# Performance work log

Measured on AMD Instinct MI355X. Metric: run time of the kernel, lower is better.

The kernel has to match this reference:

```python
import jax, jax.numpy as jnp
import numpy as np

B, S, D_IN, D_OUT = 2, 2048, 2048, 2048
NH, NKV = 16, 4
HD = D_OUT // NH          # 128
GS = NH // NKV            # 4


def _rope_tables(seq_len, head_dim, base=10000.0):
    inv = 1.0 / (base ** (np.arange(0, head_dim, 2, dtype=np.float32) / head_dim))
    t = np.arange(seq_len, dtype=np.float32)
    ang = np.outer(t, inv)                       # [S, HD/2]
    ang = np.concatenate([ang, ang], axis=-1)    # [S, HD]
    return jnp.asarray(np.cos(ang)), jnp.asarray(np.sin(ang))


def setup_inputs() -> dict:
    key = jax.random.key(0)
    ks = jax.random.split(key, 5)
    x = jax.random.normal(ks[0], (B, S, D_IN), dtype=jnp.float32)
    Wq = jax.random.normal(ks[1], (D_IN, D_OUT), dtype=jnp.float32) * 0.02
    Wk = jax.random.normal(ks[2], (D_IN, NKV * HD), dtype=jnp.float32) * 0.02
    Wv = jax.random.normal(ks[3], (D_IN, NKV * HD), dtype=jnp.float32) * 0.02
    Wo = jax.random.normal(ks[4], (D_OUT, D_OUT), dtype=jnp.float32) * 0.02
    cos, sin = _rope_tables(S, HD)
    return {"x": x, "Wq": Wq, "Wk": Wk, "Wv": Wv, "Wo": Wo, "cos": cos, "sin": sin}


def _apply_rope(t, cos, sin):
    # t: [b, h, s, hd]; cos/sin: [s, hd]
    hd = t.shape[-1]
    t1, t2 = t[..., : hd // 2], t[..., hd // 2:]
    rot = jnp.concatenate([-t2, t1], axis=-1)
    return t * cos[None, None, :, :] + rot * sin[None, None, :, :]


def reference(x, Wq, Wk, Wv, Wo, cos, sin):
    b, s, _ = x.shape
    q = (x @ Wq).reshape(b, s, NH, HD).transpose(0, 2, 1, 3)    # [b, nh, s, hd]
    k = (x @ Wk).reshape(b, s, NKV, HD).transpose(0, 2, 1, 3)   # [b, nkv, s, hd]
    v = (x @ Wv).reshape(b, s, NKV, HD).transpose(0, 2, 1, 3)
    q = _apply_rope(q, cos, sin)
    k = _apply_rope(k, cos, sin)
    # GQA: repeat_interleave kv heads to match query heads
    k = jnp.repeat(k, GS, axis=1)                               # [b, nh, s, hd]
    v = jnp.repeat(v, GS, axis=1)
    att = jnp.einsum("bhqd,bhkd->bhqk", q, k) / jnp.sqrt(jnp.float32(HD))
    causal = jnp.triu(jnp.ones((s, s), dtype=bool), k=1)         # True above diag
    att = jnp.where(causal[None, None, :, :], -jnp.inf, att)
    att = jax.nn.softmax(att, axis=-1)
    ctx = jnp.einsum("bhqk,bhkd->bhqd", att, v)                  # [b, nh, s, hd]
    ctx = ctx.transpose(0, 2, 1, 3).reshape(b, s, NH * HD)
    return ctx @ Wo
```

## Files before the change

### kernel.cpp

```cpp
#include <hip/hip_runtime.h>

#define B_ 2
#define S_ 2048
#define DIN 2048
#define DOUT 2048
#define NH 16
#define NKV 4
#define HD 128
#define QS3 3072
#define KOFF 2048
#define VOFF 2560
#define SMAX 14.0f
#define NQT 16

typedef __bf16 bf16x8 __attribute__((ext_vector_type(8)));
typedef float f32x4 __attribute__((ext_vector_type(4)));

__device__ inline unsigned short f2bf(float f) {
  union { float f; unsigned int u; } v; v.f = f;
  unsigned int r = v.u + 0x7fffu + ((v.u >> 16) & 1u);
  return (unsigned short)(r >> 16);
}
__device__ inline unsigned short f2bf_trunc(float f) {
  return (unsigned short)(__builtin_bit_cast(unsigned int, f) >> 16);
}
__device__ inline float bf2f(unsigned short h) {
  union { unsigned int u; float f; } v; v.u = ((unsigned int)h) << 16;
  return v.f;
}
__device__ inline float exp2_fast(float x) {
  float r;
  asm("v_exp_f32 %0, %1\n\ts_nop 1" : "=v"(r) : "v"(x));
  return r;
}

__device__ inline void gl_lds16(const void* g, void* l) {
  __builtin_amdgcn_global_load_lds(
      (const __attribute__((address_space(1))) void*)g,
      (__attribute__((address_space(3))) void*)l, 16, 0, 0);
}

template <int N>
__device__ inline float rrot(float v) {
  return __builtin_bit_cast(float,
      __builtin_amdgcn_update_dpp(0, __builtin_bit_cast(int, v), 0x120 | N, 0xF, 0xF, true));
}
__device__ inline float rsum16(float v) {
  v += rrot<1>(v); v += rrot<2>(v); v += rrot<4>(v); v += rrot<8>(v);
  return v;
}

__global__ __launch_bounds__(256) void cast_bf16_k(const float* __restrict__ in,
                                                   unsigned short* __restrict__ out, int n4) {
  int i = blockIdx.x * 256 + threadIdx.x;
  if (i >= n4) return;
  float4 v = ((const float4*)in)[i];
  ushort4 o;
  o.x = f2bf(v.x); o.y = f2bf(v.y); o.z = f2bf(v.z); o.w = f2bf(v.w);
  ((ushort4*)out)[i] = o;
}

__global__ void transpose_cast_k(const float* __restrict__ W, unsigned short* __restrict__ Wt,
                                 int K, int N, float scale) {
  __shared__ float tile[32][33];
  int n0 = blockIdx.x * 32, k0 = blockIdx.y * 32;
  int tx = threadIdx.x, ty = threadIdx.y;
  #pragma unroll
  for (int j = 0; j < 32; j += 8)
    tile[ty + j][tx] = W[(size_t)(k0 + ty + j) * N + n0 + tx];
  __syncthreads();
  #pragma unroll
  for (int j = 0; j < 32; j += 8)
    Wt[(size_t)(n0 + ty + j) * K + k0 + tx] = f2bf(tile[tx][ty + j] * scale);
}

__global__ void transpose_v_k(const unsigned short* __restrict__ QKV,
                              unsigned short* __restrict__ Vt) {
  __shared__ unsigned short t[32][33];
  int c0 = blockIdx.x * 32, s0 = blockIdx.y * 32, b = blockIdx.z;
  int tx = threadIdx.x, ty = threadIdx.y;
  #pragma unroll
  for (int j = 0; j < 32; j += 8)
    t[ty + j][tx] = QKV[(size_t)(b * S_ + s0 + ty + j) * QS3 + VOFF + c0 + tx];
  __syncthreads();
  #pragma unroll
  for (int j = 0; j < 32; j += 8)
    Vt[(size_t)(b * (NKV * HD) + c0 + ty + j) * S_ + s0 + tx] = t[tx][ty + j];
}

template <int OUT_BF16>
__global__ __launch_bounds__(256) void gemm_bt_k(const unsigned short* __restrict__ A,
                                                 const unsigned short* __restrict__ Bt,
                                                 void* __restrict__ Cout,
                                                 int M, int N, int K) {
  __shared__ unsigned short As[128 * 32];
  __shared__ unsigned short Bs[128 * 32];
  int tid = threadIdx.x;
  int lane = tid & 63, wave = tid >> 6;
  int wy = wave >> 1, wx = wave & 1;
  int rowA0 = blockIdx.x * 128, rowB0 = blockIdx.y * 128;
  int m16 = lane & 15, quad = lane >> 4;
  int xq = (m16 >> 1) & 3;
  f32x4 acc[4][4] = {};

  int r0 = tid >> 2, l0 = (tid & 3) ^ ((r0 >> 1) & 3);
  int c1 = 256 + tid;
  int r1 = c1 >> 2, l1 = (c1 & 3) ^ ((r1 >> 1) & 3);
  const unsigned short* pa0 = A  + (size_t)(rowA0 + r0) * K + l0 * 8;
  const unsigned short* pa1 = A  + (size_t)(rowA0 + r1) * K + l1 * 8;
  const unsigned short* pb0 = Bt + (size_t)(rowB0 + r0) * K + l0 * 8;
  const unsigned short* pb1 = Bt + (size_t)(rowB0 + r1) * K + l1 * 8;
  unsigned short* la = As + (tid & 192) * 8;
  unsigned short* lb = Bs + (tid & 192) * 8;

  for (int k0 = 0; k0 < K; k0 += 32) {
    __syncthreads();
    gl_lds16(pa0 + k0, la);
    gl_lds16(pb0 + k0, lb);
    gl_lds16(pa1 + k0, la + 2048);
    gl_lds16(pb1 + k0, lb + 2048);
    __syncthreads();
    bf16x8 af[4], bfr[4];
    #pragma unroll
    for (int i = 0; i < 4; ++i)
      af[i] = *(const bf16x8*)(As + (wy * 64 + i * 16 + m16) * 32 + (quad ^ xq) * 8);
    #pragma unroll
    for (int j = 0; j < 4; ++j)
      bfr[j] = *(const bf16x8*)(Bs + (wx * 64 + j * 16 + m16) * 32 + (quad ^ xq) * 8);
    #pragma unroll
    for (int i = 0; i < 4; ++i)
      #pragma unroll
      for (int j = 0; j < 4; ++j)
        acc[i][j] = __builtin_amdgcn_mfma_f32_16x16x32_bf16(af[i], bfr[j], acc[i][j], 0, 0, 0);
  }

  #pragma unroll
  for (int i = 0; i < 4; ++i) {
    #pragma unroll
    for (int j = 0; j < 4; ++j) {
      int row = rowA0 + wy * 64 + i * 16 + quad * 4;
      int col = rowB0 + wx * 64 + j * 16 + m16;
      #pragma unroll
      for (int r = 0; r < 4; ++r) {
        float v = acc[i][j][r];
        if (OUT_BF16)
          ((unsigned short*)Cout)[(size_t)(row + r) * N + col] = f2bf(v);
        else
          ((float*)Cout)[(size_t)(row + r) * N + col] = v;
      }
    }
  }
}

__global__ __launch_bounds__(256) void rope_k(unsigned short* __restrict__ T,
                                              const float* __restrict__ cosT,
                                              const float* __restrict__ sinT,
                                              int stride, int off, int lognh) {
  int idx = blockIdx.x * 256 + threadIdx.x;
  int d = (idx & 15) * 4;
  int t = idx >> 4;
  int nh = 1 << lognh;
  int h = t & (nh - 1);
  int bs = t >> lognh;
  int s = bs & (S_ - 1);
  unsigned short* p = T + (size_t)bs * stride + off + h * HD;
  ushort4 a = *(ushort4*)(p + d);
  ushort4 bq = *(ushort4*)(p + 64 + d);
  float4 c = *(const float4*)(cosT + s * HD + d);
  float4 sn = *(const float4*)(sinT + s * HD + d);
  ushort4 o1, o2;
  o1.x = f2bf(bf2f(a.x) * c.x - bf2f(bq.x) * sn.x);
  o2.x = f2bf(bf2f(bq.x) * c.x + bf2f(a.x) * sn.x);
  o1.y = f2bf(bf2f(a.y) * c.y - bf2f(bq.y) * sn.y);
  o2.y = f2bf(bf2f(bq.y) * c.y + bf2f(a.y) * sn.y);
  o1.z = f2bf(bf2f(a.z) * c.z - bf2f(bq.z) * sn.z);
  o2.z = f2bf(bf2f(bq.z) * c.z + bf2f(a.z) * sn.z);
  o1.w = f2bf(bf2f(a.w) * c.w - bf2f(bq.w) * sn.w);
  o2.w = f2bf(bf2f(bq.w) * c.w + bf2f(a.w) * sn.w);
  *(ushort4*)(p + d) = o1;
  *(ushort4*)(p + 64 + d) = o2;
}

#define LDP 40
__global__ __launch_bounds__(256) void flash_k(const unsigned short* __restrict__ QKV,
                                               const unsigned short* __restrict__ Vt,
                                               unsigned short* __restrict__ ctx,
                                               unsigned short* __restrict__ Opart,
                                               float* __restrict__ lpart,
                                               int CHUNK, int units_per_bh) {
  __shared__ unsigned short Ks[2][32 * 128];
  __shared__ unsigned short Vs[2][128 * 32];
  __shared__ unsigned short Ps[4][32 * LDP];
  int tid = threadIdx.x;
  int lane = tid & 63, w = tid >> 6;
  int m16 = lane & 15, quad = lane >> 4;
  int h = blockIdx.y, b = blockIdx.z;
  int g = h >> 2;

  int u = units_per_bh - 1 - (int)blockIdx.x;
  int qt = 0, prefix = 0, nc = 1;
  for (qt = 0; qt < NQT; ++qt) {
    nc = ((qt + 1) * 128 + CHUNK - 1) / CHUNK;
    if (prefix + nc > u) break;
    prefix += nc;
  }
  int ci = u - prefix;
  bool sole = (nc == 1);
  int kbeg = ci * CHUNK;
  int kend = min(kbeg + CHUNK, (qt + 1) * 128);
  int unit = (b * NH + h) * units_per_bh + u;

  bf16x8 qf[2][4];
  #pragma unroll
  for (int m = 0; m < 2; ++m) {
    int qrow = qt * 128 + w * 32 + m * 16 + m16;
    const unsigned short* Qp = QKV + (size_t)(b * S_ + qrow) * QS3 + h * HD;
    #pragma unroll
    for (int c = 0; c < 4; ++c) qf[m][c] = *(const bf16x8*)(Qp + c * 32 + quad * 8);
  }

  f32x4 o[2][8] = {};
  float lp[2][4] = {};

  int kxq = m16 & 7;
  int vxq = (m16 >> 1) & 3;

  int krow0 = tid >> 4, kcl0 = (tid & 15) ^ (krow0 & 7);
  int kc1 = 256 + tid;
  int krow1 = kc1 >> 4, kcl1 = (kc1 & 15) ^ (krow1 & 7);
  const unsigned short* kg0 = QKV + (size_t)(b * S_ + krow0) * QS3 + KOFF + g * HD + kcl0 * 8;
  const unsigned short* kg1 = QKV + (size_t)(b * S_ + krow1) * QS3 + KOFF + g * HD + kcl1 * 8;
  int vhd0 = tid >> 2, vcl0 = (tid & 3) ^ ((vhd0 >> 1) & 3);
  int vc1 = 256 + tid;
  int vhd1 = vc1 >> 2, vcl1 = (vc1 & 3) ^ ((vhd1 >> 1) & 3);
  const unsigned short* vg0 = Vt + (size_t)((b * NKV + g) * HD + vhd0) * S_ + vcl0 * 8;
  const unsigned short* vg1 = Vt + (size_t)((b * NKV + g) * HD + vhd1) * S_ + vcl1 * 8;
  int ldsoff = (tid & 192) * 8;
  unsigned short* pw = &Ps[w][0];

  gl_lds16(kg0 + (size_t)kbeg * QS3, Ks[0] + ldsoff);
  gl_lds16(kg1 + (size_t)kbeg * QS3, Ks[0] + ldsoff + 2048);
  gl_lds16(vg0 + kbeg, Vs[0] + ldsoff);
  gl_lds16(vg1 + kbeg, Vs[0] + ldsoff + 2048);
  int cur = 0;

  for (int kb = kbeg; kb < kend; kb += 32) {
    __syncthreads();
    int nkb = kb + 32;
    if (nkb < kend) {
      int nb = cur ^ 1;
      gl_lds16(kg0 + (size_t)nkb * QS3, Ks[nb] + ldsoff);
      gl_lds16(kg1 + (size_t)nkb * QS3, Ks[nb] + ldsoff + 2048);
      gl_lds16(vg0 + nkb, Vs[nb] + ldsoff);
      gl_lds16(vg1 + nkb, Vs[nb] + ldsoff + 2048);
    }
    const unsigned short* ks = Ks[cur];
    const unsigned short* vs = Vs[cur];

    f32x4 sf[2][2] = {};
    #pragma unroll
    for (int c = 0; c < 4; ++c)
      #pragma unroll
      for (int f = 0; f < 2; ++f) {
        bf16x8 kf = *(const bf16x8*)(ks + (f * 16 + m16) * 128 + ((c * 4 + quad) ^ kxq) * 8);
        sf[0][f] = __builtin_amdgcn_mfma_f32_16x16x32_bf16(qf[0][c], kf, sf[0][f], 0, 0, 0);
        sf[1][f] = __builtin_amdgcn_mfma_f32_16x16x32_bf16(qf[1][c], kf, sf[1][f], 0, 0, 0);
      }

    #pragma unroll
    for (int m = 0; m < 2; ++m) {
      int base = qt * 128 + w * 32 + m * 16;
      bool nm = (kb + 31 > base);
      #pragma unroll
      for (int r = 0; r < 4; ++r) {
        float s0 = sf[m][0][r], s1 = sf[m][1][r];
        if (nm) {
          int qr = base + quad * 4 + r;
          if (kb + m16 > qr)      s0 = -1e30f;
          if (kb + 16 + m16 > qr) s1 = -1e30f;
        }
        float p0 = exp2_fast(s0 - SMAX);
        float p1 = exp2_fast(s1 - SMAX);
        lp[m][r] += p0 + p1;
        pw[(m * 16 + quad * 4 + r) * LDP + m16]      = f2bf_trunc(p0);
        pw[(m * 16 + quad * 4 + r) * LDP + 16 + m16] = f2bf_trunc(p1);
      }
    }
    __threadfence_block();
    bf16x8 pa0 = *(const bf16x8*)(pw + m16 * LDP + quad * 8);
    bf16x8 pa1 = *(const bf16x8*)(pw + (16 + m16) * LDP + quad * 8);

    #pragma unroll
    for (int nt = 0; nt < 8; ++nt) {
      bf16x8 vf = *(const bf16x8*)(vs + (nt * 16 + m16) * 32 + (quad ^ vxq) * 8);
      o[0][nt] = __builtin_amdgcn_mfma_f32_16x16x32_bf16(pa0, vf, o[0][nt], 0, 0, 0);
      o[1][nt] = __builtin_amdgcn_mfma_f32_16x16x32_bf16(pa1, vf, o[1][nt], 0, 0, 0);
    }
    cur ^= 1;
  }

  if (sole) {
    #pragma unroll
    for (int m = 0; m < 2; ++m)
      #pragma unroll
      for (int r = 0; r < 4; ++r) {
        float inv = 1.f / rsum16(lp[m][r]);
        int row = qt * 128 + w * 32 + m * 16 + quad * 4 + r;
        #pragma unroll
        for (int nt = 0; nt < 8; ++nt)
          ctx[(size_t)(b * S_ + row) * DOUT + h * HD + nt * 16 + m16] =
              f2bf(o[m][nt][r] * inv);
      }
  } else {
    unsigned short* Op = Opart + (size_t)unit * 128 * 128;
    #pragma unroll
    for (int m = 0; m < 2; ++m)
      #pragma unroll
      for (int r = 0; r < 4; ++r) {
        int row = w * 32 + m * 16 + quad * 4 + r;
        float ls = rsum16(lp[m][r]);
        if (m16 == 0) lpart[(size_t)unit * 128 + row] = ls;
        #pragma unroll
        for (int nt = 0; nt < 8; ++nt)
          Op[row * 128 + nt * 16 + m16] = f2bf(o[m][nt][r]);
      }
  }
}

__global__ __launch_bounds__(256) void combine_k(const unsigned short* __restrict__ Opart,
                                                 const float* __restrict__ lpart,
                                                 unsigned short* __restrict__ ctx,
                                                 int CHUNK, int units_per_bh) {
  int qt = 4 + blockIdx.x, h = blockIdx.y, b = blockIdx.z;
  int prefix = 0;
  for (int j = 0; j < qt; ++j) prefix += ((j + 1) * 128 + CHUNK - 1) / CHUNK;
  int nc = ((qt + 1) * 128 + CHUNK - 1) / CHUNK;
  int unit0 = (b * NH + h) * units_per_bh + prefix;

  int tid = threadIdx.x;
  int row = tid >> 1, colb = (tid & 1) * 64;
  float denom = 0.f;
  for (int c = 0; c < nc; ++c) denom += lpart[(size_t)(unit0 + c) * 128 + row];
  float inv = 1.f / denom;

  unsigned short* dst = ctx + (size_t)(b * S_ + qt * 128 + row) * DOUT + h * HD + colb;
  for (int j = 0; j < 64; j += 8) {
    float s[8] = {};
    for (int c = 0; c < nc; ++c) {
      const unsigned short* src =
          Opart + (size_t)(unit0 + c) * 128 * 128 + row * 128 + colb + j;
      ushort4 v0 = *(const ushort4*)src;
      ushort4 v1 = *(const ushort4*)(src + 4);
      s[0] += bf2f(v0.x); s[1] += bf2f(v0.y); s[2] += bf2f(v0.z); s[3] += bf2f(v0.w);
      s[4] += bf2f(v1.x); s[5] += bf2f(v1.y); s[6] += bf2f(v1.z); s[7] += bf2f(v1.w);
    }
    ushort4 o0, o1;
    o0.x = f2bf(s[0] * inv); o0.y = f2bf(s[1] * inv);
    o0.z = f2bf(s[2] * inv); o0.w = f2bf(s[3] * inv);
    o1.x = f2bf(s[4] * inv); o1.y = f2bf(s[5] * inv);
    o1.z = f2bf(s[6] * inv); o1.w = f2bf(s[7] * inv);
    *(ushort4*)(dst + j) = o0;
    *(ushort4*)(dst + j + 4) = o1;
  }
}

extern "C" void kernel_launch(void* const* d_in, const int* in_sizes, int n_in,
                              void* d_out, int out_size, void* d_ws, size_t ws_size,
                              hipStream_t stream) {
  const float* x    = (const float*)d_in[0];
  const float* Wq   = (const float*)d_in[1];
  const float* Wk   = (const float*)d_in[2];
  const float* Wv   = (const float*)d_in[3];
  const float* Wo   = (const float*)d_in[4];
  const float* cosT = (const float*)d_in[5];
  const float* sinT = (const float*)d_in[6];

  char* ws = (char*)d_ws;
  size_t off = 0;
  auto alloc = [&](size_t bytes) { char* p = ws + off; off += bytes; return p; };
  unsigned short* xb   = (unsigned short*)alloc((size_t)B_ * S_ * DIN * 2);
  unsigned short* Wqkvt= (unsigned short*)alloc((size_t)QS3 * DIN * 2);
  unsigned short* Wot  = (unsigned short*)alloc((size_t)DOUT * DOUT * 2);
  unsigned short* QKV  = (unsigned short*)alloc((size_t)B_ * S_ * QS3 * 2);
  unsigned short* Vt   = (unsigned short*)alloc((size_t)B_ * NKV * HD * S_ * 2);
  unsigned short* ctx  = xb;

  int CHUNK = 512;
  int upb = 0;
  for (int qt = 0; qt < NQT; ++qt) upb += ((qt + 1) * 128 + CHUNK - 1) / CHUNK;
  size_t part_bytes = (size_t)B_ * NH * upb * 128 * 128 * 2;
  size_t lpart_bytes = (size_t)B_ * NH * upb * 128 * 4;
  bool split = (ws_size >= off + part_bytes + lpart_bytes);
  unsigned short* Opart = nullptr;
  float* lpartp = nullptr;
  if (split) {
    Opart = (unsigned short*)alloc(part_bytes);
    lpartp = (float*)alloc(lpart_bytes);
  } else {
    CHUNK = NQT * 128;
    upb = NQT;
    Opart = (unsigned short*)ws;
    lpartp = (float*)ws;
  }

  int M = B_ * S_;
  const float qscale = 0.08838834764831845f * 1.4426950408889634f;

  int nx4 = B_ * S_ * DIN / 4;
  cast_bf16_k<<<dim3(nx4 / 256), 256, 0, stream>>>(x, xb, nx4);

  transpose_cast_k<<<dim3(DOUT / 32, DIN / 32), dim3(32, 8), 0, stream>>>(Wq, Wqkvt, DIN, DOUT, qscale);
  transpose_cast_k<<<dim3(16, DIN / 32), dim3(32, 8), 0, stream>>>(
      Wk, Wqkvt + (size_t)KOFF * DIN, DIN, NKV * HD, 1.0f);
  transpose_cast_k<<<dim3(16, DIN / 32), dim3(32, 8), 0, stream>>>(
      Wv, Wqkvt + (size_t)VOFF * DIN, DIN, NKV * HD, 1.0f);
  transpose_cast_k<<<dim3(DOUT / 32, DOUT / 32), dim3(32, 8), 0, stream>>>(Wo, Wot, DOUT, DOUT, 1.0f);

  gemm_bt_k<1><<<dim3(M / 128, QS3 / 128), 256, 0, stream>>>(xb, Wqkvt, QKV, M, QS3, DIN);

  rope_k<<<dim3(B_ * S_ * NH * 16 / 256), 256, 0, stream>>>(QKV, cosT, sinT, QS3, 0, 4);
  rope_k<<<dim3(B_ * S_ * NKV * 16 / 256), 256, 0, stream>>>(QKV, cosT, sinT, QS3, KOFF, 2);

  transpose_v_k<<<dim3(16, S_ / 32, B_), dim3(32, 8), 0, stream>>>(QKV, Vt);

  flash_k<<<dim3(upb, NH, B_), 256, 0, stream>>>(QKV, Vt, ctx, Opart, lpartp, CHUNK, upb);
  if (split)
    combine_k<<<dim3(NQT - 4, NH, B_), 256, 0, stream>>>(Opart, lpartp, ctx, CHUNK, upb);

  gemm_bt_k<0><<<dim3(M / 128, DOUT / 128), 256, 0, stream>>>(ctx, Wot, d_out, M, DOUT, DIN);
}
```

Measured before the change: 370.6 us.

## Process two KV tiles per iteration with four-slot LDS ring buffer

The flash attention loop now stages K/V tiles into a four-slot LDS ring and handles two 32-key tiles per iteration. Both QK^T products are issued before the softmax/PV work so MFMA and exp work can interleave, and there is one block barrier per two tiles instead of one per tile. It also swaps the inline-asm exp for the compiler builtin and drops the threadfence_block before reading P back from LDS. The change doubles K/V LDS usage, which may lower occupancy, and it assumes the tile count per chunk is even.

```diff
diff --git a/kernel.cpp b/kernel.cpp
--- a/kernel.cpp
+++ b/kernel.cpp
@@ -28,11 +28,15 @@
   union { unsigned int u; float f; } v; v.u = ((unsigned int)h) << 16;
   return v.f;
 }
+#if __has_builtin(__builtin_amdgcn_exp2f)
+__device__ inline float exp2_fast(float x) { return __builtin_amdgcn_exp2f(x); }
+#else
 __device__ inline float exp2_fast(float x) {
   float r;
   asm("v_exp_f32 %0, %1\n\ts_nop 1" : "=v"(r) : "v"(x));
   return r;
 }
+#endif
 
 __device__ inline void gl_lds16(const void* g, void* l) {
   __builtin_amdgcn_global_load_lds(
@@ -188,8 +192,8 @@
                                                unsigned short* __restrict__ Opart,
                                                float* __restrict__ lpart,
                                                int CHUNK, int units_per_bh) {
-  __shared__ unsigned short Ks[2][32 * 128];
-  __shared__ unsigned short Vs[2][128 * 32];
+  __shared__ unsigned short Ks4[4][32 * 128];
+  __shared__ unsigned short Vs4[4][128 * 32];
   __shared__ unsigned short Ps[4][32 * LDP];
   int tid = threadIdx.x;
   int lane = tid & 63, w = tid >> 6;
@@ -208,6 +212,7 @@
   bool sole = (nc == 1);
   int kbeg = ci * CHUNK;
   int kend = min(kbeg + CHUNK, (qt + 1) * 128);
+  int ntiles = (kend - kbeg) >> 5;
   int unit = (b * NH + h) * units_per_bh + u;
 
   bf16x8 qf[2][4];
@@ -238,26 +243,16 @@
   int ldsoff = (tid & 192) * 8;
   unsigned short* pw = &Ps[w][0];
 
-  gl_lds16(kg0 + (size_t)kbeg * QS3, Ks[0] + ldsoff);
-  gl_lds16(kg1 + (size_t)kbeg * QS3, Ks[0] + ldsoff + 2048);
-  gl_lds16(vg0 + kbeg, Vs[0] + ldsoff);
-  gl_lds16(vg1 + kbeg, Vs[0] + ldsoff + 2048);
-  int cur = 0;
-
-  for (int kb = kbeg; kb < kend; kb += 32) {
-    __syncthreads();
-    int nkb = kb + 32;
-    if (nkb < kend) {
-      int nb = cur ^ 1;
-      gl_lds16(kg0 + (size_t)nkb * QS3, Ks[nb] + ldsoff);
-      gl_lds16(kg1 + (size_t)nkb * QS3, Ks[nb] + ldsoff + 2048);
-      gl_lds16(vg0 + nkb, Vs[nb] + ldsoff);
-      gl_lds16(vg1 + nkb, Vs[nb] + ldsoff + 2048);
-    }
-    const unsigned short* ks = Ks[cur];
-    const unsigned short* vs = Vs[cur];
-
-    f32x4 sf[2][2] = {};
+  auto stage = [&](int t) {
+    int kb = kbeg + t * 32;
+    int sl = t & 3;
+    gl_lds16(kg0 + (size_t)kb * QS3, Ks4[sl] + ldsoff);
+    gl_lds16(kg1 + (size_t)kb * QS3, Ks4[sl] + ldsoff + 2048);
+    gl_lds16(vg0 + kb, Vs4[sl] + ldsoff);
+    gl_lds16(vg1 + kb, Vs4[sl] + ldsoff + 2048);
+  };
+
+  auto qk_tile = [&](const unsigned short* ks, f32x4 (&sf)[2][2]) {
     #pragma unroll
     for (int c = 0; c < 4; ++c)
       #pragma unroll
@@ -266,7 +261,9 @@
         sf[0][f] = __builtin_amdgcn_mfma_f32_16x16x32_bf16(qf[0][c], kf, sf[0][f], 0, 0, 0);
         sf[1][f] = __builtin_amdgcn_mfma_f32_16x16x32_bf16(qf[1][c], kf, sf[1][f], 0, 0, 0);
       }
-
+  };
+
+  auto sm_pv = [&](f32x4 (&sf)[2][2], int kb, const unsigned short* vs) {
     #pragma unroll
     for (int m = 0; m < 2; ++m) {
       int base = qt * 128 + w * 32 + m * 16;
@@ -286,17 +283,28 @@
         pw[(m * 16 + quad * 4 + r) * LDP + 16 + m16] = f2bf_trunc(p1);
       }
     }
-    __threadfence_block();
     bf16x8 pa0 = *(const bf16x8*)(pw + m16 * LDP + quad * 8);
     bf16x8 pa1 = *(const bf16x8*)(pw + (16 + m16) * LDP + quad * 8);
-
     #pragma unroll
     for (int nt = 0; nt < 8; ++nt) {
       bf16x8 vf = *(const bf16x8*)(vs + (nt * 16 + m16) * 32 + (quad ^ vxq) * 8);
       o[0][nt] = __builtin_amdgcn_mfma_f32_16x16x32_bf16(pa0, vf, o[0][nt], 0, 0, 0);
       o[1][nt] = __builtin_amdgcn_mfma_f32_16x16x32_bf16(pa1, vf, o[1][nt], 0, 0, 0);
     }
-    cur ^= 1;
+  };
+
+  stage(0);
+  stage(1);
+
+  for (int tp = 0; tp < ntiles; tp += 2) {
+    __syncthreads();
+    if (tp + 2 < ntiles) { stage(tp + 2); stage(tp + 3); }
+    int sa = tp & 3, sb = (tp + 1) & 3;
+    f32x4 sfa[2][2] = {}, sfb[2][2] = {};
+    qk_tile(Ks4[sa], sfa);
+    qk_tile(Ks4[sb], sfb);
+    sm_pv(sfa, kbeg + tp * 32, Vs4[sa]);
+    sm_pv(sfb, kbeg + tp * 32 + 32, Vs4[sb]);
   }
 
   if (sole) {
```

Result: faster. 363.0 us (-2.1%).
